# Performance work log

Measured on AMD Instinct MI355X. Metric: run time of the kernel, lower is better.

Reference implementation:

```python
import jax, jax.numpy as jnp
import numpy as np

HC = 32  # half_color_channels


def dwconv(x, w, padding):
    # depthwise conv, NCHW / OIHW, groups == channels
    return jax.lax.conv_general_dilated(
        x, w, (1, 1), padding,
        feature_group_count=x.shape[1],
        dimension_numbers=('NCHW', 'OIHW', 'NCHW'))


def setup_inputs() -> dict:
    key = jax.random.key(0)
    ks = jax.random.split(key, 6)
    B, C, H, W = 8, 2 * HC, 256, 256
    mask = jax.random.normal(ks[0], (B, 8, 16, 16), dtype=jnp.float32)  # unused by forward math
    color = jax.random.normal(ks[1], (B, C, H, W), dtype=jnp.float32)
    w_bbx = jax.random.normal(ks[2], (C, 1, 1, 1), dtype=jnp.float32) * 0.2
    w_width = jax.random.normal(ks[3], (HC, 1, 1, 5), dtype=jnp.float32) * 0.2
    w_height = jax.random.normal(ks[4], (HC, 1, 5, 1), dtype=jnp.float32) * 0.2
    w_score = jax.random.normal(ks[5], (1, C, 1, 1), dtype=jnp.float32) * 0.05
    return {"mask": mask, "color": color, "w_bbx": w_bbx,
            "w_width": w_width, "w_height": w_height, "w_score": w_score}


def _forward(color, w_bbx, w_width, w_height, w_score):
    B, C, H, W = color.shape
    # depthwise 1x1 conv == per-channel scale
    wh = color * w_bbx[:, 0, 0, 0][None, :, None, None]
    # even channels -> horizontal (1,5) depthwise, odd -> vertical (5,1) depthwise; max over channels
    wmap = dwconv(wh[:, 0::2], w_width, ((0, 0), (2, 2))).max(axis=1, keepdims=True)
    hmap = dwconv(wh[:, 1::2], w_height, ((2, 2), (0, 0))).max(axis=1, keepdims=True)
    # dense 1x1 conv on the raw input for the score channel
    score = jnp.einsum('bchw,oc->bohw', color, w_score[:, :, 0, 0])
    bbx = jnp.concatenate([score, wmap, hmap], axis=1)  # [B,3,H,W]
    bf = bbx.transpose(0, 2, 3, 1).reshape(B, -1, 3)    # [B,HW,3]
    s = jax.nn.sigmoid(bf[:, :, 0])                      # [B,HW]
    wv = bf[:, :, 0]  # NOTE: faithful to original code, which reuses channel 0 for w
    hv = bf[:, :, 1]  #       and channel 1 for h
    # top-10 per image, then threshold masking
    _, ti = jax.lax.top_k(s, 10)                         # [B,10]
    m = jnp.zeros_like(s, dtype=bool).at[jnp.arange(B)[:, None], ti].set(True)
    m = (m & (s > 0.6)) | (s > 0.8)                      # [B,HW] selection mask
    # coordinate grids in flattened H-major order
    yg = jnp.repeat(jnp.arange(H, dtype=s.dtype), W)[None, :]  # [1,HW]
    xg = jnp.tile(jnp.arange(W, dtype=s.dtype), H)[None, :]
    cw = jnp.exp(wv) * 10.0
    ch = jnp.exp(hv) * 10.0
    x1 = jnp.floor(xg - cw); x2 = jnp.ceil(xg + cw)
    y1 = jnp.floor(yg - ch); y2 = jnp.ceil(yg + ch)
    # clamp out-of-bounds boxes symmetrically around the center
    bad = (x1 < 0) | (x2 > W)
    hw = jnp.minimum(W - xg, xg)
    x1 = jnp.where(bad, jnp.floor(xg - hw), x1)
    x2 = jnp.where(bad, jnp.ceil(xg + hw), x2)
    bad = (y1 < 0) | (y2 > H)
    hh = jnp.minimum(H - yg, yg)
    y1 = jnp.where(bad, jnp.floor(yg - hh), y1)
    y2 = jnp.where(bad, jnp.ceil(yg + hh), y2)
    # dense padded equivalent of boolean compaction: zero out unselected rows
    out = jnp.stack([s, x1, y1, x2, y2], axis=-1) * m[..., None]  # [B,HW,5]
    return score, out, m


def reference(mask, color, w_bbx, w_width, w_height, w_score):
    return _forward(color, w_bbx, w_width, w_height, w_score)
```

## Files before the change

kernel.cpp:

```cpp
#include <hip/hip_runtime.h>
#include <math.h>


__device__ __forceinline__ void merge10(float (&a)[10], const float (&b)[10]) {
    float c[10];
#pragma unroll
    for (int k = 0; k < 10; ++k) {
        float best = fmaxf(a[k], b[k]);
#pragma unroll
        for (int i = 0; i < k; ++i) best = fmaxf(best, fminf(a[i], b[k - 1 - i]));
        c[k] = best;
    }
#pragma unroll
    for (int k = 0; k < 10; ++k) a[k] = c[k];
}

__global__ __launch_bounds__(256, 4) void k_main(
    const float* __restrict__ color,
    const float* __restrict__ w_bbx,
    const float* __restrict__ w_width,
    const float* __restrict__ w_score,
    float* __restrict__ score_out,
    float* __restrict__ wmap_out,
    float* __restrict__ lists)
{
    const int tid  = threadIdx.x;
    const int lane = tid & 63;
    const int wid  = tid >> 6;
    const int bid  = blockIdx.x;
    const int b    = bid >> 8;
    const int h    = bid & 255;
    const int w0   = lane << 2;

    const int cg = __builtin_amdgcn_readfirstlane(wid) << 4;

    const float* base = color + ((size_t)b << 22) + ((size_t)h << 8) + (size_t)w0
                              + ((size_t)cg << 16);

    float a0 = 0.f, a1 = 0.f, a2 = 0.f, a3 = 0.f;
    float m0 = -INFINITY, m1 = -INFINITY, m2 = -INFINITY, m3 = -INFINITY;

#pragma unroll
    for (int cc = 0; cc < 16; cc += 2) {
        const float4 v = *reinterpret_cast<const float4*>(base + ((size_t)cc << 16));
        const float4 u = *reinterpret_cast<const float4*>(base + ((size_t)(cc + 1) << 16));
        const int c = cg + cc;
        const float wsc0 = w_score[c];
        const float wsc1 = w_score[c + 1];
        a0 += v.x * wsc0 + u.x * wsc1;
        a1 += v.y * wsc0 + u.y * wsc1;
        a2 += v.z * wsc0 + u.z * wsc1;
        a3 += v.w * wsc0 + u.w * wsc1;

        const float wb = w_bbx[c];
        const float ex = v.x * wb, ey = v.y * wb, ez = v.z * wb, ew = v.w * wb;
        float lm2 = __shfl_up(ez, 1);
        float lm1 = __shfl_up(ew, 1);
        float rp1 = __shfl_down(ex, 1);
        float rp2 = __shfl_down(ey, 1);
        if (lane == 0)  { lm2 = 0.f; lm1 = 0.f; }
        if (lane == 63) { rp1 = 0.f; rp2 = 0.f; }

        const int hc = c >> 1;
        const float t0 = w_width[hc * 5 + 0];
        const float t1 = w_width[hc * 5 + 1];
        const float t2 = w_width[hc * 5 + 2];
        const float t3 = w_width[hc * 5 + 3];
        const float t4 = w_width[hc * 5 + 4];

        m0 = fmaxf(m0, lm2 * t0 + lm1 * t1 + ex * t2 + ey * t3 + ez * t4);
        m1 = fmaxf(m1, lm1 * t0 + ex * t1 + ey * t2 + ez * t3 + ew * t4);
        m2 = fmaxf(m2, ex * t0 + ey * t1 + ez * t2 + ew * t3 + rp1 * t4);
        m3 = fmaxf(m3, ey * t0 + ez * t1 + ew * t2 + rp1 * t3 + rp2 * t4);
    }

    __shared__ float sa[4][256];
    __shared__ float sm[4][256];
    *reinterpret_cast<float4*>(&sa[wid][w0]) = make_float4(a0, a1, a2, a3);
    *reinterpret_cast<float4*>(&sm[wid][w0]) = make_float4(m0, m1, m2, m3);
    __syncthreads();

    const float s = (sa[0][tid] + sa[1][tid]) + (sa[2][tid] + sa[3][tid]);
    const float m = fmaxf(fmaxf(sm[0][tid], sm[1][tid]), fmaxf(sm[2][tid], sm[3][tid]));
    const size_t o = ((size_t)b << 16) + ((size_t)h << 8) + (size_t)tid;
    score_out[o] = s;
    wmap_out[o]  = m;

    float t10[10];
    t10[0] = s;
#pragma unroll
    for (int k = 1; k < 10; ++k) t10[k] = -INFINITY;

#pragma unroll
    for (int off = 1; off < 64; off <<= 1) {
        float b10[10];
#pragma unroll
        for (int k = 0; k < 10; ++k) b10[k] = __shfl_xor(t10[k], off);
        merge10(t10, b10);
    }

    __shared__ float wl[4][10];
    if (lane == 0) {
#pragma unroll
        for (int k = 0; k < 10; ++k) wl[wid][k] = t10[k];
    }
    __syncthreads();

    if (tid == 0) {
        float fa[10], fb[10];
#pragma unroll
        for (int k = 0; k < 10; ++k) fa[k] = wl[0][k];
#pragma unroll
        for (int k = 0; k < 10; ++k) fb[k] = wl[1][k];
        merge10(fa, fb);
#pragma unroll
        for (int k = 0; k < 10; ++k) fb[k] = wl[2][k];
        merge10(fa, fb);
#pragma unroll
        for (int k = 0; k < 10; ++k) fb[k] = wl[3][k];
        merge10(fa, fb);
#pragma unroll
        for (int k = 0; k < 10; ++k) lists[bid * 10 + k] = fa[k];
    }
}

__global__ __launch_bounds__(256) void k_boxes(
    const float* __restrict__ score,
    const float* __restrict__ lists,
    float* __restrict__ out5,
    float* __restrict__ mout)
{
    const int tid = threadIdx.x;
    const int i   = blockIdx.x * 256 + tid;
    const int b   = i >> 16;
    const int pix = i & 65535;

    const float sc = score[i];
    const float wm = mout[i];

    __shared__ float tbs;
    if (tid < 64) {
        const float* p = lists + ((size_t)b << 8) * 10;
        float a[10];
#pragma unroll
        for (int k = 0; k < 10; ++k) a[k] = p[tid * 10 + k];
#pragma unroll
        for (int j = 1; j < 4; ++j) {
            float t[10];
#pragma unroll
            for (int k = 0; k < 10; ++k) t[k] = p[(tid + 64 * j) * 10 + k];
            merge10(a, t);
        }
#pragma unroll
        for (int off = 1; off < 64; off <<= 1) {
            float b10[10];
#pragma unroll
            for (int k = 0; k < 10; ++k) b10[k] = __shfl_xor(a[k], off);
            merge10(a, b10);
        }
        if (tid == 0) tbs = a[9];
    }
    __syncthreads();
    const float tb = tbs;

    const double sd  = 1.0 / (1.0 + exp(-(double)sc));
    const bool  top  = (sc >= tb);
    const bool  m    = (top && (sd > 0.6)) || (sd > 0.8);

    const double xg = (double)(pix & 255);
    const double yg = (double)(pix >> 8);
    const double cw = exp((double)sc) * 10.0;
    const double ch = exp((double)wm) * 10.0;

    double x1 = floor(xg - cw), x2 = ceil(xg + cw);
    double y1 = floor(yg - ch), y2 = ceil(yg + ch);
    if ((x1 < 0.0) || (x2 > 256.0)) {
        const double hw = fmin(256.0 - xg, xg);
        x1 = floor(xg - hw); x2 = ceil(xg + hw);
    }
    if ((y1 < 0.0) || (y2 > 256.0)) {
        const double hh = fmin(256.0 - yg, yg);
        y1 = floor(yg - hh); y2 = ceil(yg + hh);
    }

    const float mf = m ? 1.0f : 0.0f;
    const size_t o = (size_t)i * 5;
    out5[o + 0] = mf * (float)sd;
    out5[o + 1] = mf * (float)x1;
    out5[o + 2] = mf * (float)y1;
    out5[o + 3] = mf * (float)x2;
    out5[o + 4] = mf * (float)y2;
    mout[i] = mf;
}

extern "C" void kernel_launch(void* const* d_in, const int* in_sizes, int n_in,
                              void* d_out, int out_size, void* d_ws, size_t ws_size,
                              hipStream_t stream) {
    const float* color   = (const float*)d_in[1];
    const float* w_bbx   = (const float*)d_in[2];
    const float* w_width = (const float*)d_in[3];
    const float* w_score = (const float*)d_in[5];

    float* score_out = (float*)d_out;
    float* out5      = score_out + 524288;
    float* mout      = score_out + 524288 + 2621440;

    float* lists = (float*)d_ws;

    k_main <<<2048, 256, 0, stream>>>(color, w_bbx, w_width, w_score, score_out, mout, lists);
    k_boxes<<<2048, 256, 0, stream>>>(score_out, lists, out5, mout);
}
```

Baseline: 213.4 us.

## Fuse main and box kernels via per-image atomic counter and spin-wait flag

Merges the conv/score kernel and the box kernel into one launch of 512 blocks, each handling four rows. The last block per image merges the top-10 lists and publishes a threshold through a flag that the other blocks spin-wait on. Score and wmap values stay in shared memory, so the wmap round trip through global memory and the second launch are gone. Top-10 shuffles are also size-templated so early merge rounds do less work. The spin-wait depends on all 64 blocks of an image being co-resident, which holds only if the whole grid fits on the device at once, and it adds a memset launch.

Measured after the change: 329.3 us. 1.54x slower.

```diff
diff --git a/kernel.cpp b/kernel.cpp
--- a/kernel.cpp
+++ b/kernel.cpp
@@ -2,107 +2,151 @@
 #include <math.h>
 
 
-__device__ __forceinline__ void merge10(float (&a)[10], const float (&b)[10]) {
+template<int NA, int NB>
+__device__ __forceinline__ void merge_sz(float (&a)[10], const float (&b)[10]) {
+    constexpr int NC = (NA + NB < 10) ? (NA + NB) : 10;
     float c[10];
 #pragma unroll
-    for (int k = 0; k < 10; ++k) {
-        float best = fmaxf(a[k], b[k]);
-#pragma unroll
-        for (int i = 0; i < k; ++i) best = fmaxf(best, fminf(a[i], b[k - 1 - i]));
+    for (int k = 0; k < NC; ++k) {
+        float best = (k < NA) ? a[k] : -INFINITY;
+        if (k < NB) best = fmaxf(best, b[k]);
+#pragma unroll
+        for (int i = 0; i < NA; ++i) {
+            const int j = k - 1 - i;
+            if (j >= 0 && j < NB) best = fmaxf(best, fminf(a[i], b[j]));
+        }
         c[k] = best;
     }
 #pragma unroll
-    for (int k = 0; k < 10; ++k) a[k] = c[k];
-}
-
-__global__ __launch_bounds__(256, 4) void k_main(
+    for (int k = 0; k < NC; ++k) a[k] = c[k];
+}
+
+__device__ __forceinline__ void wave_top10(float s, float (&t)[10]) {
+    t[0] = s;
+#pragma unroll
+    for (int k = 1; k < 10; ++k) t[k] = -INFINITY;
+    float bt[10];
+#pragma unroll
+    for (int k = 0; k < 10; ++k) bt[k] = -INFINITY;
+
+    bt[0] = __shfl_xor(t[0], 1);
+    merge_sz<1, 1>(t, bt);
+#pragma unroll
+    for (int k = 0; k < 2; ++k) bt[k] = __shfl_xor(t[k], 2);
+    merge_sz<2, 2>(t, bt);
+#pragma unroll
+    for (int k = 0; k < 4; ++k) bt[k] = __shfl_xor(t[k], 4);
+    merge_sz<4, 4>(t, bt);
+#pragma unroll
+    for (int k = 0; k < 8; ++k) bt[k] = __shfl_xor(t[k], 8);
+    merge_sz<8, 8>(t, bt);
+#pragma unroll
+    for (int k = 0; k < 10; ++k) bt[k] = __shfl_xor(t[k], 16);
+    merge_sz<10, 10>(t, bt);
+#pragma unroll
+    for (int k = 0; k < 10; ++k) bt[k] = __shfl_xor(t[k], 32);
+    merge_sz<10, 10>(t, bt);
+}
+
+__global__ __launch_bounds__(256, 2) void k_all(
     const float* __restrict__ color,
     const float* __restrict__ w_bbx,
     const float* __restrict__ w_width,
     const float* __restrict__ w_score,
     float* __restrict__ score_out,
-    float* __restrict__ wmap_out,
+    float* __restrict__ out5,
+    float* __restrict__ mout,
+    int*   __restrict__ cnt,
+    int*   __restrict__ flag,
+    float* __restrict__ tvals,
     float* __restrict__ lists)
 {
     const int tid  = threadIdx.x;
     const int lane = tid & 63;
     const int wid  = tid >> 6;
     const int bid  = blockIdx.x;
-    const int b    = bid >> 8;
-    const int h    = bid & 255;
+    const int b    = bid >> 6;
+    const int rg   = bid & 63;
     const int w0   = lane << 2;
 
-    const int cg = __builtin_amdgcn_readfirstlane(wid) << 4;
-
-    const float* base = color + ((size_t)b << 22) + ((size_t)h << 8) + (size_t)w0
-                              + ((size_t)cg << 16);
-
-    float a0 = 0.f, a1 = 0.f, a2 = 0.f, a3 = 0.f;
-    float m0 = -INFINITY, m1 = -INFINITY, m2 = -INFINITY, m3 = -INFINITY;
-
-#pragma unroll
-    for (int cc = 0; cc < 16; cc += 2) {
-        const float4 v = *reinterpret_cast<const float4*>(base + ((size_t)cc << 16));
-        const float4 u = *reinterpret_cast<const float4*>(base + ((size_t)(cc + 1) << 16));
-        const int c = cg + cc;
-        const float wsc0 = w_score[c];
-        const float wsc1 = w_score[c + 1];
-        a0 += v.x * wsc0 + u.x * wsc1;
-        a1 += v.y * wsc0 + u.y * wsc1;
-        a2 += v.z * wsc0 + u.z * wsc1;
-        a3 += v.w * wsc0 + u.w * wsc1;
-
-        const float wb = w_bbx[c];
-        const float ex = v.x * wb, ey = v.y * wb, ez = v.z * wb, ew = v.w * wb;
-        float lm2 = __shfl_up(ez, 1);
-        float lm1 = __shfl_up(ew, 1);
-        float rp1 = __shfl_down(ex, 1);
-        float rp2 = __shfl_down(ey, 1);
-        if (lane == 0)  { lm2 = 0.f; lm1 = 0.f; }
-        if (lane == 63) { rp1 = 0.f; rp2 = 0.f; }
-
-        const int hc = c >> 1;
-        const float t0 = w_width[hc * 5 + 0];
-        const float t1 = w_width[hc * 5 + 1];
-        const float t2 = w_width[hc * 5 + 2];
-        const float t3 = w_width[hc * 5 + 3];
-        const float t4 = w_width[hc * 5 + 4];
-
-        m0 = fmaxf(m0, lm2 * t0 + lm1 * t1 + ex * t2 + ey * t3 + ez * t4);
-        m1 = fmaxf(m1, lm1 * t0 + ex * t1 + ey * t2 + ez * t3 + ew * t4);
-        m2 = fmaxf(m2, ex * t0 + ey * t1 + ez * t2 + ew * t3 + rp1 * t4);
-        m3 = fmaxf(m3, ey * t0 + ez * t1 + ew * t2 + rp1 * t3 + rp2 * t4);
-    }
+    const int cgr = __builtin_amdgcn_readfirstlane(wid) << 4;
 
     __shared__ float sa[4][256];
     __shared__ float sm[4][256];
-    *reinterpret_cast<float4*>(&sa[wid][w0]) = make_float4(a0, a1, a2, a3);
-    *reinterpret_cast<float4*>(&sm[wid][w0]) = make_float4(m0, m1, m2, m3);
-    __syncthreads();
-
-    const float s = (sa[0][tid] + sa[1][tid]) + (sa[2][tid] + sa[3][tid]);
-    const float m = fmaxf(fmaxf(sm[0][tid], sm[1][tid]), fmaxf(sm[2][tid], sm[3][tid]));
-    const size_t o = ((size_t)b << 16) + ((size_t)h << 8) + (size_t)tid;
-    score_out[o] = s;
-    wmap_out[o]  = m;
-
-    float t10[10];
-    t10[0] = s;
-#pragma unroll
-    for (int k = 1; k < 10; ++k) t10[k] = -INFINITY;
-
-#pragma unroll
-    for (int off = 1; off < 64; off <<= 1) {
-        float b10[10];
-#pragma unroll
-        for (int k = 0; k < 10; ++k) b10[k] = __shfl_xor(t10[k], off);
-        merge10(t10, b10);
-    }
-
+    __shared__ float sfin[4][256];
+    __shared__ float mfin[4][256];
     __shared__ float wl[4][10];
+    __shared__ int   last_s;
+    __shared__ float tb_s;
+
+    float run10[10];
+
+    for (int r = 0; r < 4; ++r) {
+        const int h = (rg << 2) + r;
+        const float* base = color + ((size_t)b << 22) + ((size_t)h << 8) + (size_t)w0
+                                  + ((size_t)cgr << 16);
+
+        float a0 = 0.f, a1 = 0.f, a2 = 0.f, a3 = 0.f;
+        float m0 = -INFINITY, m1 = -INFINITY, m2 = -INFINITY, m3 = -INFINITY;
+
+#pragma unroll
+        for (int cc = 0; cc < 16; cc += 2) {
+            const float4 v = *reinterpret_cast<const float4*>(base + ((size_t)cc << 16));
+            const float4 u = *reinterpret_cast<const float4*>(base + ((size_t)(cc + 1) << 16));
+            const int c = cgr + cc;
+            const float wsc0 = w_score[c];
+            const float wsc1 = w_score[c + 1];
+            a0 += v.x * wsc0 + u.x * wsc1;
+            a1 += v.y * wsc0 + u.y * wsc1;
+            a2 += v.z * wsc0 + u.z * wsc1;
+            a3 += v.w * wsc0 + u.w * wsc1;
+
+            const float wb = w_bbx[c];
+            const float ex = v.x * wb, ey = v.y * wb, ez = v.z * wb, ew = v.w * wb;
+            float lm2 = __shfl_up(ez, 1);
+            float lm1 = __shfl_up(ew, 1);
+            float rp1 = __shfl_down(ex, 1);
+            float rp2 = __shfl_down(ey, 1);
+            if (lane == 0)  { lm2 = 0.f; lm1 = 0.f; }
+            if (lane == 63) { rp1 = 0.f; rp2 = 0.f; }
+
+            const int hc = c >> 1;
+            const float t0 = w_width[hc * 5 + 0];
+            const float t1 = w_width[hc * 5 + 1];
+            const float t2 = w_width[hc * 5 + 2];
+            const float t3 = w_width[hc * 5 + 3];
+            const float t4 = w_width[hc * 5 + 4];
+
+            m0 = fmaxf(m0, lm2 * t0 + lm1 * t1 + ex * t2 + ey * t3 + ez * t4);
+            m1 = fmaxf(m1, lm1 * t0 + ex * t1 + ey * t2 + ez * t3 + ew * t4);
+            m2 = fmaxf(m2, ex * t0 + ey * t1 + ez * t2 + ew * t3 + rp1 * t4);
+            m3 = fmaxf(m3, ey * t0 + ez * t1 + ew * t2 + rp1 * t3 + rp2 * t4);
+        }
+
+        if (r) __syncthreads();
+        *reinterpret_cast<float4*>(&sa[wid][w0]) = make_float4(a0, a1, a2, a3);
+        *reinterpret_cast<float4*>(&sm[wid][w0]) = make_float4(m0, m1, m2, m3);
+        __syncthreads();
+
+        const float s = (sa[0][tid] + sa[1][tid]) + (sa[2][tid] + sa[3][tid]);
+        const float m = fmaxf(fmaxf(sm[0][tid], sm[1][tid]), fmaxf(sm[2][tid], sm[3][tid]));
+        sfin[r][tid] = s;
+        mfin[r][tid] = m;
+        score_out[((size_t)b << 16) + ((size_t)h << 8) + (size_t)tid] = s;
+
+        float t10[10];
+        wave_top10(s, t10);
+        if (r == 0) {
+#pragma unroll
+            for (int k = 0; k < 10; ++k) run10[k] = t10[k];
+        } else {
+            merge_sz<10, 10>(run10, t10);
+        }
+    }
+
     if (lane == 0) {
 #pragma unroll
-        for (int k = 0; k < 10; ++k) wl[wid][k] = t10[k];
+        for (int k = 0; k < 10; ++k) wl[wid][k] = run10[k];
     }
     __syncthreads();
 
@@ -112,85 +156,89 @@
         for (int k = 0; k < 10; ++k) fa[k] = wl[0][k];
 #pragma unroll
         for (int k = 0; k < 10; ++k) fb[k] = wl[1][k];
-        merge10(fa, fb);
+        merge_sz<10, 10>(fa, fb);
 #pragma unroll
         for (int k = 0; k < 10; ++k) fb[k] = wl[2][k];
-        merge10(fa, fb);
+        merge_sz<10, 10>(fa, fb);
 #pragma unroll
         for (int k = 0; k < 10; ++k) fb[k] = wl[3][k];
-        merge10(fa, fb);
+        merge_sz<10, 10>(fa, fb);
 #pragma unroll
         for (int k = 0; k < 10; ++k) lists[bid * 10 + k] = fa[k];
-    }
-}
-
-__global__ __launch_bounds__(256) void k_boxes(
-    const float* __restrict__ score,
-    const float* __restrict__ lists,
-    float* __restrict__ out5,
-    float* __restrict__ mout)
-{
-    const int tid = threadIdx.x;
-    const int i   = blockIdx.x * 256 + tid;
-    const int b   = i >> 16;
-    const int pix = i & 65535;
-
-    const float sc = score[i];
-    const float wm = mout[i];
-
-    __shared__ float tbs;
-    if (tid < 64) {
-        const float* p = lists + ((size_t)b << 8) * 10;
+
+        __threadfence();
+        const int ticket = __hip_atomic_fetch_add(&cnt[b], 1, __ATOMIC_ACQ_REL,
+                                                  __HIP_MEMORY_SCOPE_AGENT);
+        last_s = (ticket == 63) ? 1 : 0;
+    }
+    __syncthreads();
+
+    if (last_s && wid == 0) {
+        __threadfence();
+        const float* p = lists + ((size_t)b << 6) * 10;
         float a[10];
 #pragma unroll
-        for (int k = 0; k < 10; ++k) a[k] = p[tid * 10 + k];
-#pragma unroll
-        for (int j = 1; j < 4; ++j) {
-            float t[10];
-#pragma unroll
-            for (int k = 0; k < 10; ++k) t[k] = p[(tid + 64 * j) * 10 + k];
-            merge10(a, t);
-        }
+        for (int k = 0; k < 10; ++k) a[k] = p[lane * 10 + k];
+        float bt[10];
 #pragma unroll
         for (int off = 1; off < 64; off <<= 1) {
-            float b10[10];
-#pragma unroll
-            for (int k = 0; k < 10; ++k) b10[k] = __shfl_xor(a[k], off);
-            merge10(a, b10);
-        }
-        if (tid == 0) tbs = a[9];
+#pragma unroll
+            for (int k = 0; k < 10; ++k) bt[k] = __shfl_xor(a[k], off);
+            merge_sz<10, 10>(a, bt);
+        }
+        if (lane == 0) {
+            tvals[b] = a[9];
+            __threadfence();
+            __hip_atomic_store(&flag[b], 1, __ATOMIC_RELEASE, __HIP_MEMORY_SCOPE_AGENT);
+        }
+    }
+
+    if (tid == 0) {
+        while (__hip_atomic_load(&flag[b], __ATOMIC_ACQUIRE,
+                                 __HIP_MEMORY_SCOPE_AGENT) == 0) {
+            __builtin_amdgcn_s_sleep(4);
+        }
+        __threadfence();
+        tb_s = tvals[b];
     }
     __syncthreads();
-    const float tb = tbs;
-
-    const double sd  = 1.0 / (1.0 + exp(-(double)sc));
-    const bool  top  = (sc >= tb);
-    const bool  m    = (top && (sd > 0.6)) || (sd > 0.8);
-
-    const double xg = (double)(pix & 255);
-    const double yg = (double)(pix >> 8);
-    const double cw = exp((double)sc) * 10.0;
-    const double ch = exp((double)wm) * 10.0;
-
-    double x1 = floor(xg - cw), x2 = ceil(xg + cw);
-    double y1 = floor(yg - ch), y2 = ceil(yg + ch);
-    if ((x1 < 0.0) || (x2 > 256.0)) {
-        const double hw = fmin(256.0 - xg, xg);
-        x1 = floor(xg - hw); x2 = ceil(xg + hw);
-    }
-    if ((y1 < 0.0) || (y2 > 256.0)) {
-        const double hh = fmin(256.0 - yg, yg);
-        y1 = floor(yg - hh); y2 = ceil(yg + hh);
-    }
-
-    const float mf = m ? 1.0f : 0.0f;
-    const size_t o = (size_t)i * 5;
-    out5[o + 0] = mf * (float)sd;
-    out5[o + 1] = mf * (float)x1;
-    out5[o + 2] = mf * (float)y1;
-    out5[o + 3] = mf * (float)x2;
-    out5[o + 4] = mf * (float)y2;
-    mout[i] = mf;
+    const float tb = tb_s;
+
+    for (int r = 0; r < 4; ++r) {
+        const int h  = (rg << 2) + r;
+        const int i  = (b << 16) | (h << 8) | tid;
+        const float sc = sfin[r][tid];
+        const float wm = mfin[r][tid];
+
+        const double sd = 1.0 / (1.0 + exp(-(double)sc));
+        const bool top  = (sc >= tb);
+        const bool m    = (top && (sd > 0.6)) || (sd > 0.8);
+
+        const double xg = (double)(i & 255);
+        const double yg = (double)((i >> 8) & 255);
+        const double cw = exp((double)sc) * 10.0;
+        const double ch = exp((double)wm) * 10.0;
+
+        double x1 = floor(xg - cw), x2 = ceil(xg + cw);
+        double y1 = floor(yg - ch), y2 = ceil(yg + ch);
+        if ((x1 < 0.0) || (x2 > 256.0)) {
+            const double hw = fmin(256.0 - xg, xg);
+            x1 = floor(xg - hw); x2 = ceil(xg + hw);
+        }
+        if ((y1 < 0.0) || (y2 > 256.0)) {
+            const double hh = fmin(256.0 - yg, yg);
+            y1 = floor(yg - hh); y2 = ceil(yg + hh);
+        }
+
+        const float mf = m ? 1.0f : 0.0f;
+        const size_t o = (size_t)i * 5;
+        out5[o + 0] = mf * (float)sd;
+        out5[o + 1] = mf * (float)x1;
+        out5[o + 2] = mf * (float)y1;
+        out5[o + 3] = mf * (float)x2;
+        out5[o + 4] = mf * (float)y2;
+        mout[i] = mf;
+    }
 }
 
 extern "C" void kernel_launch(void* const* d_in, const int* in_sizes, int n_in,
@@ -205,8 +253,15 @@
     float* out5      = score_out + 524288;
     float* mout      = score_out + 524288 + 2621440;
 
-    float* lists = (float*)d_ws;
-
-    k_main <<<2048, 256, 0, stream>>>(color, w_bbx, w_width, w_score, score_out, mout, lists);
-    k_boxes<<<2048, 256, 0, stream>>>(score_out, lists, out5, mout);
-}
+    int*   cnt   = (int*)d_ws;
+    int*   flagp = cnt + 8;
+    float* tvals = (float*)(flagp + 8);
+    float* lists = tvals + 8;
+
+    hipMemsetAsync(d_ws, 0, 64, stream);
+
+    void* args_unused = nullptr; (void)args_unused;
+    k_all<<<512, 256, 0, stream>>>(color, w_bbx, w_width, w_score,
+                                   score_out, out5, mout,
+                                   cnt, flagp, tvals, lists);
+}
```
